# Performance work log

Measured on AMD Instinct MI355X. Metric: run time of the kernel, lower is better.

The kernel has to match this reference:

```python
import jax, jax.numpy as jnp
import numpy as np

B, H, S, D = 2, 16, 2048, 64

def setup_inputs() -> dict:
    key = jax.random.key(0)
    kq, kk, kv = jax.random.split(key, 3)
    Q = jax.random.normal(kq, (B, H, S, D), dtype=jnp.float32)
    K = jax.random.normal(kk, (B, H, S, D), dtype=jnp.float32)
    V = jax.random.normal(kv, (B, H, S, D), dtype=jnp.float32)
    # causal mask, broadcastable over batch and heads
    mask = jnp.tril(jnp.ones((S, S), dtype=bool))[None, None, :, :]
    return {"Q": Q, "K": K, "V": V, "mask": mask}

def reference(Q, K, V, mask):
    # scores: [B,H,S,S]
    scores = jnp.einsum('bhqd,bhkd->bhqk', Q, K)
    # original applies mask (-inf) BEFORE scaling; -inf/scale == -inf so math matches
    scores = jnp.where(mask, scores, -jnp.inf)
    scores = scores / jnp.sqrt(jnp.float32(K.shape[-1]))
    attn = jax.nn.softmax(scores, axis=-1)
    return jnp.einsum('bhqk,bhkd->bhqd', attn, V)
```

## Files before the change

### kernel.cpp

```cpp
#include <hip/hip_runtime.h>

#define SEQ 2048
#define HD  64
#define SCALE 0.18033688011111772f

typedef __bf16 bf16x8 __attribute__((ext_vector_type(8)));
typedef __bf16 bf16x4 __attribute__((ext_vector_type(4)));
typedef __bf16 bf16x2 __attribute__((ext_vector_type(2)));
typedef float  f32x4  __attribute__((ext_vector_type(4)));
typedef float  f32x16 __attribute__((ext_vector_type(16)));

#define BAR_LGKM() asm volatile("s_waitcnt lgkmcnt(0)\n\ts_barrier" ::: "memory")

union PU { unsigned u[4]; bf16x8 v; };

__device__ __forceinline__ unsigned pk2(float lo, float hi) {
    union { unsigned u; bf16x2 v; } t;
    t.v = bf16x2{(__bf16)lo, (__bf16)hi};
    return t.u;
}

__device__ __forceinline__ void plswap(unsigned &x, unsigned &y) {
#if __has_builtin(__builtin_amdgcn_permlane32_swap)
    auto r = __builtin_amdgcn_permlane32_swap(x, y, false, false);
    x = (unsigned)r[0];
    y = (unsigned)r[1];
#else
    asm("v_permlane32_swap_b32 %0, %1" : "+v"(x), "+v"(y));
#endif
}

__global__ __launch_bounds__(512, 2) void attn_fwd(
    const float* __restrict__ Q,
    const float* __restrict__ K,
    const float* __restrict__ V,
    float* __restrict__ O)
{
    __shared__ __align__(16) unsigned char smem[33792];
    #define KBp(kh,b,key,c8) ((__bf16*)(smem +         (((kh)<<13) + ((b)<<12) + ((key)<<7) + ((c8)<<4))))
    #define VTp(kh,b,r,c8)   ((__bf16*)(smem + 16384 + (((kh)<<13) + ((b)<<12) + ((r)<<6)   + ((c8)<<4))))

    const int tid  = threadIdx.x;
    const int wave = tid >> 6;
    const int lane = tid & 63;
    const int n    = lane & 31;
    const int p    = lane >> 5;
    const int w3   = wave & 3;
    const int kh   = wave >> 2;

    const int x  = blockIdx.x;
    const int bh = x & 31;
    const int sr = x >> 5;
    const int s  = (sr & 8) ? (15 - (sr & 7)) : sr;

    const int R0   = s * 128 + w3 * 32;
    const int span = 4 * s + w3;
    const int jmax = 2 * s + 2;
    const int tB   = kh * jmax;

    const float* __restrict__ Qh = Q + (size_t)bh * SEQ * HD;
    const float* __restrict__ Kh = K + (size_t)bh * SEQ * HD;
    const float* __restrict__ Vh = V + (size_t)bh * SEQ * HD;
    float* __restrict__       Oh = O + (size_t)bh * SEQ * HD;

    bf16x8 qf[4];
    {
        const float* qrow = Qh + (size_t)(R0 + n) * HD;
        #pragma unroll
        for (int c = 0; c < 4; ++c) {
            f32x4 a = *(const f32x4*)(qrow + 16 * c + 8 * p);
            f32x4 b = *(const f32x4*)(qrow + 16 * c + 8 * p + 4);
            #pragma unroll
            for (int j = 0; j < 4; ++j) {
                qf[c][j]     = (__bf16)(a[j] * SCALE);
                qf[c][4 + j] = (__bf16)(b[j] * SCALE);
            }
        }
    }

    f32x16 oT[2] = {};
    float  l_own = 0.f;

    const int sg    = tid >> 8;
    const int t8    = tid & 255;
    const int key_s = t8 >> 3;
    const int dgi8  = t8 & 7;
    const int swk   = key_s & 7;
    const int Ls    = t8 & 31;
    const int ko    = t8 >> 5;
    const int swv   = Ls & 3;
    const int ku    = ko >> 1;
    const int khalf = ko & 1;

    const float* kbase = Kh + (size_t)key_s * HD + dgi8 * 8;
    const float* vbase = Vh + (size_t)(ko * 4) * HD + 2 * Ls;

    f32x4  kst[2];
    float2 vst[4];

    auto loadt = [&](int j) {
        const size_t off = (size_t)(32 * (sg * jmax + j)) * HD;
        const float* kp = kbase + off;
        kst[0] = *(const f32x4*)(kp);
        kst[1] = *(const f32x4*)(kp + 4);
        const float* vp = vbase + off;
        #pragma unroll
        for (int jj = 0; jj < 4; ++jj) vst[jj] = *(const float2*)(vp + (size_t)jj * HD);
    };

    auto stage = [&](int b) {
        bf16x8 w0;
        #pragma unroll
        for (int j = 0; j < 4; ++j) { w0[j] = (__bf16)kst[0][j]; w0[4 + j] = (__bf16)kst[1][j]; }
        *(bf16x8*)KBp(sg, b, key_s, dgi8 ^ swk) = w0;

        bf16x4 v0, v1;
        #pragma unroll
        for (int j = 0; j < 4; ++j) { v0[j] = (__bf16)vst[j].x; v1[j] = (__bf16)vst[j].y; }
        *(bf16x4*)(VTp(sg, b, 2 * Ls,     ku ^ swv) + 4 * khalf) = v0;
        *(bf16x4*)(VTp(sg, b, 2 * Ls + 1, ku ^ swv) + 4 * khalf) = v1;
    };

    loadt(0);
    stage(0);
    loadt(1);

    #pragma unroll 1
    for (int j = 0; j < jmax; ++j) {
        BAR_LGKM();
        const int cur = j & 1;
        const int T   = tB + j;

        if (T <= span) {
            __builtin_amdgcn_s_setprio(1);
            f32x16 sT = {};
            #pragma unroll
            for (int cc = 0; cc < 4; ++cc) {
                bf16x8 kf = *(const bf16x8*)KBp(kh, cur, n, (2 * cc + p) ^ (n & 7));
                sT = __builtin_amdgcn_mfma_f32_32x32x16_bf16(kf, qf[cc], sT, 0, 0, 0);
            }

            const bool diag = (T == span);
            float ts = 0.f;
            #pragma unroll
            for (int r = 0; r < 16; ++r) {
                float pe = __builtin_amdgcn_exp2f(sT[r]);
                if (diag) {
                    const int kk = (r & 3) + 8 * (r >> 2) + 4 * p;
                    pe = (kk <= n) ? pe : 0.f;
                }
                sT[r] = pe;
                ts += pe;
            }
            l_own += ts;

            unsigned a0 = pk2(sT[0],  sT[1]),  a1 = pk2(sT[2],  sT[3]);
            unsigned a2 = pk2(sT[4],  sT[5]),  a3 = pk2(sT[6],  sT[7]);
            unsigned b0 = pk2(sT[8],  sT[9]),  b1 = pk2(sT[10], sT[11]);
            unsigned b2 = pk2(sT[12], sT[13]), b3 = pk2(sT[14], sT[15]);
            plswap(a0, a2);
            plswap(a1, a3);
            plswap(b0, b2);
            plswap(b1, b3);
            PU pu0, pu1;
            pu0.u[0] = a0; pu0.u[1] = a1; pu0.u[2] = a2; pu0.u[3] = a3;
            pu1.u[0] = b0; pu1.u[1] = b1; pu1.u[2] = b2; pu1.u[3] = b3;
            bf16x8 pf0 = pu0.v;
            bf16x8 pf1 = pu1.v;

            const int swn = (n >> 1) & 3;
            #pragma unroll
            for (int dg = 0; dg < 2; ++dg) {
                bf16x8 vf0 = *(const bf16x8*)VTp(kh, cur, 32 * dg + n, p ^ swn);
                bf16x8 vf1 = *(const bf16x8*)VTp(kh, cur, 32 * dg + n, (2 + p) ^ swn);
                oT[dg] = __builtin_amdgcn_mfma_f32_32x32x16_bf16(vf0, pf0, oT[dg], 0, 0, 0);
                oT[dg] = __builtin_amdgcn_mfma_f32_32x32x16_bf16(vf1, pf1, oT[dg], 0, 0, 0);
            }
            __builtin_amdgcn_s_setprio(0);
        }

        if (j + 1 < jmax) stage(cur ^ 1);
        if (j + 2 < jmax) loadt(j + 2);
    }

    float l_part = l_own + __shfl_xor(l_own, 32, 64);

    __syncthreads();
    float* Os = (float*)smem;
    const int cb = w3 * 2112;

    if (kh == 1) {
        #pragma unroll
        for (int dg = 0; dg < 2; ++dg)
            #pragma unroll
            for (int r = 0; r < 16; ++r)
                Os[cb + (dg * 16 + r) * 64 + lane] = oT[dg][r];
        Os[cb + 2048 + lane] = l_part;
    }
    __syncthreads();
    if (kh == 0) {
        const float linv = 1.0f / (l_part + Os[cb + 2048 + lane]);
        #pragma unroll
        for (int dg = 0; dg < 2; ++dg) {
            #pragma unroll
            for (int u4 = 0; u4 < 4; ++u4) {
                f32x4 o;
                #pragma unroll
                for (int j = 0; j < 4; ++j) {
                    const int r = 4 * u4 + j;
                    o[j] = (oT[dg][r] + Os[cb + (dg * 16 + r) * 64 + lane]) * linv;
                }
                *(f32x4*)&Oh[(size_t)(R0 + n) * HD + dg * 32 + u4 * 8 + 4 * p] = o;
            }
        }
    }
}

extern "C" void kernel_launch(void* const* d_in, const int* in_sizes, int n_in,
                              void* d_out, int out_size, void* d_ws, size_t ws_size,
                              hipStream_t stream) {
    const float* Q = (const float*)d_in[0];
    const float* K = (const float*)d_in[1];
    const float* V = (const float*)d_in[2];
    float* O = (float*)d_out;

    dim3 grid(512);
    dim3 block(512);
    attn_fwd<<<grid, block, 0, stream>>>(Q, K, V, O);
}
```

Baseline: 125.4 us.

## Split key range across four wave groups with 1024-thread blocks

Doubles the block to 1024 threads so four wave groups, instead of two, each take an interleaved quarter of the key tiles. Each group now handles tiles 4j+kq. LDS doubles to 64KB to hold per-group K/V double buffers. The final reduction merges three partial O/l sets through shared memory in two phases. The aim is to shorten the serial key loop per block, at the cost of more LDS, a heavier reduction, and possibly lower occupancy (two 1024-thread blocks per CU with 64KB each).

```diff
diff --git a/kernel.cpp b/kernel.cpp
--- a/kernel.cpp
+++ b/kernel.cpp
@@ -30,15 +30,15 @@
 #endif
 }
 
-__global__ __launch_bounds__(512, 2) void attn_fwd(
+__global__ __launch_bounds__(1024, 2) void attn_fwd(
     const float* __restrict__ Q,
     const float* __restrict__ K,
     const float* __restrict__ V,
     float* __restrict__ O)
 {
-    __shared__ __align__(16) unsigned char smem[33792];
-    #define KBp(kh,b,key,c8) ((__bf16*)(smem +         (((kh)<<13) + ((b)<<12) + ((key)<<7) + ((c8)<<4))))
-    #define VTp(kh,b,r,c8)   ((__bf16*)(smem + 16384 + (((kh)<<13) + ((b)<<12) + ((r)<<6)   + ((c8)<<4))))
+    __shared__ __align__(16) unsigned char smem[65536];
+    #define KBp(kq,b,key,c8) ((__bf16*)(smem +         (((kq)<<13) + ((b)<<12) + ((key)<<7) + ((c8)<<4))))
+    #define VTp(kq,b,r,c8)   ((__bf16*)(smem + 32768 + (((kq)<<13) + ((b)<<12) + ((r)<<6)   + ((c8)<<4))))
 
     const int tid  = threadIdx.x;
     const int wave = tid >> 6;
@@ -46,7 +46,7 @@
     const int n    = lane & 31;
     const int p    = lane >> 5;
     const int w3   = wave & 3;
-    const int kh   = wave >> 2;
+    const int kq   = wave >> 2;
 
     const int x  = blockIdx.x;
     const int bh = x & 31;
@@ -55,8 +55,7 @@
 
     const int R0   = s * 128 + w3 * 32;
     const int span = 4 * s + w3;
-    const int jmax = 2 * s + 2;
-    const int tB   = kh * jmax;
+    const int jmax = s + 1;
 
     const float* __restrict__ Qh = Q + (size_t)bh * SEQ * HD;
     const float* __restrict__ Kh = K + (size_t)bh * SEQ * HD;
@@ -99,7 +98,7 @@
     float2 vst[4];
 
     auto loadt = [&](int j) {
-        const size_t off = (size_t)(32 * (sg * jmax + j)) * HD;
+        const size_t off = (size_t)(32 * (4 * j + sg)) * HD;
         const float* kp = kbase + off;
         kst[0] = *(const f32x4*)(kp);
         kst[1] = *(const f32x4*)(kp + 4);
@@ -123,20 +122,20 @@
 
     loadt(0);
     stage(0);
-    loadt(1);
+    if (1 < jmax) loadt(1);
 
     #pragma unroll 1
     for (int j = 0; j < jmax; ++j) {
         BAR_LGKM();
         const int cur = j & 1;
-        const int T   = tB + j;
+        const int T   = 4 * j + kq;
 
         if (T <= span) {
             __builtin_amdgcn_s_setprio(1);
             f32x16 sT = {};
             #pragma unroll
             for (int cc = 0; cc < 4; ++cc) {
-                bf16x8 kf = *(const bf16x8*)KBp(kh, cur, n, (2 * cc + p) ^ (n & 7));
+                bf16x8 kf = *(const bf16x8*)KBp(kq, cur, n, (2 * cc + p) ^ (n & 7));
                 sT = __builtin_amdgcn_mfma_f32_32x32x16_bf16(kf, qf[cc], sT, 0, 0, 0);
             }
 
@@ -171,8 +170,8 @@
             const int swn = (n >> 1) & 3;
             #pragma unroll
             for (int dg = 0; dg < 2; ++dg) {
-                bf16x8 vf0 = *(const bf16x8*)VTp(kh, cur, 32 * dg + n, p ^ swn);
-                bf16x8 vf1 = *(const bf16x8*)VTp(kh, cur, 32 * dg + n, (2 + p) ^ swn);
+                bf16x8 vf0 = *(const bf16x8*)VTp(kq, cur, 32 * dg + n, p ^ swn);
+                bf16x8 vf1 = *(const bf16x8*)VTp(kq, cur, 32 * dg + n, (2 + p) ^ swn);
                 oT[dg] = __builtin_amdgcn_mfma_f32_32x32x16_bf16(vf0, pf0, oT[dg], 0, 0, 0);
                 oT[dg] = __builtin_amdgcn_mfma_f32_32x32x16_bf16(vf1, pf1, oT[dg], 0, 0, 0);
             }
@@ -184,33 +183,43 @@
     }
 
     float l_part = l_own + __shfl_xor(l_own, 32, 64);
-
-    __syncthreads();
     float* Os = (float*)smem;
-    const int cb = w3 * 2112;
-
-    if (kh == 1) {
-        #pragma unroll
-        for (int dg = 0; dg < 2; ++dg)
-            #pragma unroll
-            for (int r = 0; r < 16; ++r)
-                Os[cb + (dg * 16 + r) * 64 + lane] = oT[dg][r];
-        Os[cb + 2048 + lane] = l_part;
-    }
-    __syncthreads();
-    if (kh == 0) {
-        const float linv = 1.0f / (l_part + Os[cb + 2048 + lane]);
-        #pragma unroll
-        for (int dg = 0; dg < 2; ++dg) {
-            #pragma unroll
-            for (int u4 = 0; u4 < 4; ++u4) {
-                f32x4 o;
+
+    #pragma unroll 1
+    for (int ph = 0; ph < 2; ++ph) {
+        __syncthreads();
+        const int sl = w3 - 2 * ph;
+        if (sl == 0 || sl == 1) {
+            if (kq != 0) {
+                float* dst = Os + (sl * 3 + (kq - 1)) * 2112;
                 #pragma unroll
-                for (int j = 0; j < 4; ++j) {
-                    const int r = 4 * u4 + j;
-                    o[j] = (oT[dg][r] + Os[cb + (dg * 16 + r) * 64 + lane]) * linv;
+                for (int dg = 0; dg < 2; ++dg)
+                    #pragma unroll
+                    for (int r = 0; r < 16; ++r)
+                        dst[(dg * 16 + r) * 64 + lane] = oT[dg][r];
+                dst[2048 + lane] = l_part;
+            }
+        }
+        __syncthreads();
+        if ((sl == 0 || sl == 1) && kq == 0) {
+            float* s0 = Os + (sl * 3 + 0) * 2112;
+            float* s1 = Os + (sl * 3 + 1) * 2112;
+            float* s2 = Os + (sl * 3 + 2) * 2112;
+            const float lsum = l_part + s0[2048 + lane] + s1[2048 + lane] + s2[2048 + lane];
+            const float linv = 1.0f / lsum;
+            #pragma unroll
+            for (int dg = 0; dg < 2; ++dg) {
+                #pragma unroll
+                for (int u4 = 0; u4 < 4; ++u4) {
+                    f32x4 o;
+                    #pragma unroll
+                    for (int j = 0; j < 4; ++j) {
+                        const int r   = 4 * u4 + j;
+                        const int idx = (dg * 16 + r) * 64 + lane;
+                        o[j] = (oT[dg][r] + s0[idx] + s1[idx] + s2[idx]) * linv;
+                    }
+                    *(f32x4*)&Oh[(size_t)(R0 + n) * HD + dg * 32 + u4 * 8 + 4 * p] = o;
                 }
-                *(f32x4*)&Oh[(size_t)(R0 + n) * HD + dg * 32 + u4 * 8 + 4 * p] = o;
             }
         }
     }
@@ -225,6 +234,6 @@
     float* O = (float*)d_out;
 
     dim3 grid(512);
-    dim3 block(512);
+    dim3 block(1024);
     attn_fwd<<<grid, block, 0, stream>>>(Q, K, V, O);
 }
```

Result: slower. 128.7 us (+2.6%).
